# Kernel optimization log

Measured on AMD Instinct MI355X. Metric: run time of the kernel, lower is better.

The kernel has to match this reference:

```python
import jax, jax.numpy as jnp
import numpy as np

CONV_SPECS = [(1, 64, 4, 2), (64, 128, 8, 4), (128, 256, 10, 5), (256, 256, 12, 6)]  # (cin, cout, k, stride)
N_CODEBOOKS = 8
CODEBOOK_SIZE = 1024
D_MODEL = 256
STATE_FRAMES = 4
B = 8192


def setup_inputs() -> dict:
    key = jax.random.key(0)
    ks = jax.random.split(key, 3 + 2 * len(CONV_SPECS) + 1)
    d = {
        "audio_frame": jax.random.normal(ks[0], (B, 1, 240), dtype=jnp.float32),
        "state_in": jax.random.normal(ks[1], (B, D_MODEL, STATE_FRAMES), dtype=jnp.float32),
    }
    for i, (cin, cout, k, s) in enumerate(CONV_SPECS):
        scale = 1.0 / np.sqrt(cin * k)
        d[f"W{i}"] = jax.random.normal(ks[2 + 2 * i], (cout, cin, k), dtype=jnp.float32) * scale
        d[f"b{i}"] = jnp.zeros((cout,), dtype=jnp.float32)
    d["codebooks"] = jax.random.normal(ks[-1], (N_CODEBOOKS, CODEBOOK_SIZE, D_MODEL), dtype=jnp.float32) * 0.02
    return d


def _causal_conv(x, W, b, stride):
    # x: [B, Cin, L]; causal left-pad of (k - stride) so L_out = L // stride
    k = W.shape[-1]
    x = jnp.pad(x, ((0, 0), (0, 0), (k - stride, 0)))
    y = jax.lax.conv_general_dilated(
        x, W, window_strides=(stride,), padding="VALID",
        dimension_numbers=("NCH", "OIH", "NCH"))
    return y + b[None, :, None]


def _rvq_indices(x_btd, codebooks):
    # x_btd: [B, T, D]; codebooks: [Q, K, D] -> indices [B, Q, T]
    r = x_btd
    idxs = []
    for q in range(codebooks.shape[0]):
        cb = codebooks[q]                                        # [K, D]
        # ||r - c||^2 = ||r||^2 - 2 r.c + ||c||^2 ; ||r||^2 constant over k for argmin
        dist = jnp.sum(cb * cb, axis=-1) - 2.0 * jnp.einsum("btd,kd->btk", r, cb)
        idx = jnp.argmin(dist, axis=-1)                          # [B, T]
        r = r - cb[idx]                                          # residual update
        idxs.append(idx)
    return jnp.stack(idxs, axis=1)                               # [B, Q, T]


def reference(audio_frame, state_in, W0, b0, W1, b1, W2, b2, W3, b3, codebooks):
    # state: roll left, zero last frame
    new_state = jnp.roll(state_in, -1, axis=2).at[:, :, -1].set(0.0)

    # causal conv encoder stack (ELU between conv blocks)
    Ws, bs = (W0, W1, W2, W3), (b0, b1, b2, b3)
    x = audio_frame
    for i, (_, _, _, stride) in enumerate(CONV_SPECS):
        x = _causal_conv(x, Ws[i], bs[i], stride)
        if i < len(CONV_SPECS) - 1:
            x = jax.nn.elu(x)
    # x: [B, D_MODEL, 1]

    new_state = new_state.at[:, :, -1].set(x[:, :, -1])

    z = _rvq_indices(x.transpose(0, 2, 1), codebooks)            # [B, Q, T]
    acoustic_tokens = z[:, :, -1]                                # [B, 8]
    return acoustic_tokens, new_state
```

## Files before the change

### kernel.cpp

```cpp
#include <hip/hip_runtime.h>
#include <hip/hip_bf16.h>

#define GB 2

__device__ __forceinline__ float elu1(float v) { return v > 0.f ? v : expm1f(v); }

__global__ void cnorm_kernel(const float* __restrict__ cb, float* __restrict__ cnorm) {
    int g = blockIdx.x * blockDim.x + threadIdx.x;
    if (g >= 8 * 1024) return;
    const float* p = cb + (size_t)g * 256;
    float s = 0.f;
    for (int d = 0; d < 256; d += 4) {
        float4 v = *reinterpret_cast<const float4*>(p + d);
        s += v.x * v.x + v.y * v.y + v.z * v.z + v.w * v.w;
    }
    cnorm[g] = s;
}

__global__ void cbtrans_kernel(const float* __restrict__ cb, float* __restrict__ cbT) {
    int t = blockIdx.x * blockDim.x + threadIdx.x;
    int o = t * 4;
    const int s = o >> 13;
    const int r = o & 8191;
    const int dl = r >> 10;
    const int k = r & 1023;
    const int q = s >> 5;
    const int d = (s & 31) * 8 + dl;
    const float* src = cb + ((size_t)(q * 1024 + k)) * 256 + d;
    float4 v;
    v.x = src[0 * 256]; v.y = src[1 * 256]; v.z = src[2 * 256]; v.w = src[3 * 256];
    *reinterpret_cast<float4*>(cbT + o) = v;
}

__global__ void wtrans_kernel(const float* __restrict__ W1, const float* __restrict__ W2,
                              const float* __restrict__ W3, float* __restrict__ W1T,
                              float* __restrict__ W2T, float* __restrict__ W3T) {
    int g = blockIdx.x * blockDim.x + threadIdx.x;
    if (g < 8192) {
        int ci = g >> 7, c = g & 127;
        const float* src = W1 + c * 512 + ci * 8;
        float4 a = *reinterpret_cast<const float4*>(src);
        float4 b = *reinterpret_cast<const float4*>(src + 4);
        *reinterpret_cast<float4*>(W1T + g * 8) = a;
        *reinterpret_cast<float4*>(W1T + g * 8 + 4) = b;
    }
    int g2 = g - 8192;
    if (g2 >= 0 && g2 < 32768) {
        int ci = g2 >> 8, c = g2 & 255;
        const float* src = W2 + c * 1280 + ci * 10;
        float* dst = W2T + g2 * 10;
#pragma unroll
        for (int j = 0; j < 5; ++j)
            *reinterpret_cast<float2*>(dst + 2 * j) =
                *reinterpret_cast<const float2*>(src + 2 * j);
    }
    int g3 = g - 40960;
    if (g3 >= 0 && g3 < 65536) {
        int ci = g3 >> 8, c = g3 & 255;
        const float* src = W3 + c * 3072 + ci * 12 + 6;
        float* dst = W3T + g3 * 6;
#pragma unroll
        for (int j = 0; j < 3; ++j)
            *reinterpret_cast<float2*>(dst + 2 * j) =
                *reinterpret_cast<const float2*>(src + 2 * j);
    }
}

__global__ __launch_bounds__(256, 2)
void convA_kernel(const float* __restrict__ audio,
                  const float* __restrict__ W0, const float* __restrict__ b0,
                  const float* __restrict__ W1T, const float* __restrict__ b1,
                  float* __restrict__ y1g) {
    __shared__ __align__(16) float xs[244];
    __shared__ __align__(16) float y0s[64 * 124];

    const int tid = threadIdx.x;
    const int b = blockIdx.x;

    if (tid < 64) {
        y0s[tid * 124 + 0] = 0.f; y0s[tid * 124 + 1] = 0.f;
        y0s[tid * 124 + 2] = 0.f; y0s[tid * 124 + 3] = 0.f;
    }
    if (tid < 242) xs[tid] = (tid < 2) ? 0.f : audio[b * 240 + tid - 2];
    __syncthreads();
    {
        const int ci = tid >> 2, tg = tid & 3;
        float4 w = *reinterpret_cast<const float4*>(W0 + ci * 4);
        float bias = b0[ci];
        for (int t = tg; t < 120; t += 4) {
            float v = bias + w.x * xs[2 * t] + w.y * xs[2 * t + 1]
                           + w.z * xs[2 * t + 2] + w.w * xs[2 * t + 3];
            y0s[ci * 124 + 4 + t] = elu1(v);
        }
    }
    __syncthreads();
    {
        const int c = tid >> 1, half = tid & 1, t0 = 15 * half;
        float acc[15];
        float bias = b1[c];
#pragma unroll
        for (int u = 0; u < 15; ++u) acc[u] = bias;
        const float* wbase = W1T + c * 8;
        for (int ci = 0; ci < 64; ++ci) {
            float4 wA = *reinterpret_cast<const float4*>(wbase + ci * 1024);
            float4 wB = *reinterpret_cast<const float4*>(wbase + ci * 1024 + 4);
            const float* yb = y0s + ci * 124 + 4 * t0;
#pragma unroll
            for (int u = 0; u < 15; ++u) {
                float4 a = *reinterpret_cast<const float4*>(yb + 4 * u);
                float4 d = *reinterpret_cast<const float4*>(yb + 4 * u + 4);
                acc[u] += wA.x * a.x + wA.y * a.y + wA.z * a.z + wA.w * a.w
                        + wB.x * d.x + wB.y * d.y + wB.z * d.z + wB.w * d.w;
            }
        }
        float* yo = y1g + ((size_t)b * 128 + c) * 32 + t0;
#pragma unroll
        for (int u = 0; u < 15; ++u) yo[u] = elu1(acc[u]);
    }
}

__global__ __launch_bounds__(256, 2)
void convB_kernel(const float* __restrict__ state_in,
                  const float* __restrict__ b2, const float* __restrict__ b3,
                  const float* __restrict__ W2T, const float* __restrict__ W3T,
                  const float* __restrict__ y1g,
                  float* __restrict__ out, float* __restrict__ r_ws) {
    __shared__ __align__(16) float y1s[GB * 128 * 32];
    __shared__ __align__(16) float y2s[GB * 256 * 6];

    const int tid = threadIdx.x;
    const int bbase = blockIdx.x * GB;

    {
        const int col = tid & 31, grp = tid >> 5;
#pragma unroll
        for (int bi = 0; bi < GB; ++bi) {
            const float* src = y1g + ((size_t)(bbase + bi) * 128 + grp * 16) * 32 + col;
            float* dst = y1s + (bi * 128 + grp * 16) * 32 + col;
#pragma unroll
            for (int i = 0; i < 16; ++i) dst[i * 32] = src[i * 32];
        }
    }
    __syncthreads();
    {
        const int c = tid;
        float acc[GB][6];
        float bias = b2[c];
#pragma unroll
        for (int bi = 0; bi < GB; ++bi)
#pragma unroll
            for (int t = 0; t < 6; ++t) acc[bi][t] = bias;
        const float* wbase = W2T + c * 10;
        for (int ci = 0; ci < 128; ++ci) {
            float w[10];
#pragma unroll
            for (int jj = 0; jj < 5; ++jj) {
                float2 wv = *reinterpret_cast<const float2*>(wbase + ci * 2560 + jj * 2);
                w[jj * 2] = wv.x; w[jj * 2 + 1] = wv.y;
            }
#pragma unroll
            for (int bi = 0; bi < GB; ++bi) {
                const float* yr = y1s + (bi * 128 + ci) * 32;
                float row[32];
#pragma unroll
                for (int k4 = 0; k4 < 8; ++k4) {
                    float4 v = *reinterpret_cast<const float4*>(yr + k4 * 4);
                    row[k4 * 4] = v.x; row[k4 * 4 + 1] = v.y;
                    row[k4 * 4 + 2] = v.z; row[k4 * 4 + 3] = v.w;
                }
                acc[bi][0] += w[5] * row[0] + w[6] * row[1] + w[7] * row[2]
                            + w[8] * row[3] + w[9] * row[4];
#pragma unroll
                for (int t = 1; t < 6; ++t) {
                    const int q0 = 5 * t - 5;
                    float s = 0.f;
#pragma unroll
                    for (int j = 0; j < 10; ++j) s += w[j] * row[q0 + j];
                    acc[bi][t] += s;
                }
            }
        }
#pragma unroll
        for (int bi = 0; bi < GB; ++bi)
#pragma unroll
            for (int t = 0; t < 6; ++t)
                y2s[(bi * 256 + c) * 6 + t] = elu1(acc[bi][t]);
    }
    __syncthreads();
    {
        const int c = tid;
        float acc[GB];
        float bias = b3[c];
#pragma unroll
        for (int bi = 0; bi < GB; ++bi) acc[bi] = bias;
        const float* wbase = W3T + c * 6;
        for (int ci = 0; ci < 256; ++ci) {
            float2 w01 = *reinterpret_cast<const float2*>(wbase + ci * 1536);
            float2 w23 = *reinterpret_cast<const float2*>(wbase + ci * 1536 + 2);
            float2 w45 = *reinterpret_cast<const float2*>(wbase + ci * 1536 + 4);
#pragma unroll
            for (int bi = 0; bi < GB; ++bi) {
                const float* yr = y2s + (bi * 256 + ci) * 6;
                float2 a = *reinterpret_cast<const float2*>(yr);
                float2 d = *reinterpret_cast<const float2*>(yr + 2);
                float2 e = *reinterpret_cast<const float2*>(yr + 4);
                acc[bi] += w01.x * a.x + w01.y * a.y + w23.x * d.x + w23.y * d.y
                         + w45.x * e.x + w45.y * e.y;
            }
        }
#pragma unroll
        for (int bi = 0; bi < GB; ++bi) {
            const int b = bbase + bi;
            float y3 = acc[bi];
            r_ws[b * 256 + c] = y3;
            float4 si = *reinterpret_cast<const float4*>(state_in + b * 1024 + c * 4);
            float4 o; o.x = si.y; o.y = si.z; o.z = si.w; o.w = y3;
            *reinterpret_cast<float4*>(out + 65536 + b * 1024 + c * 4) = o;
        }
    }
}

__device__ __forceinline__ unsigned long long distkey(float d, int k) {
    unsigned u = __float_as_uint(d);
    u = (u & 0x80000000u) ? ~u : (u | 0x80000000u);
    return ((unsigned long long)u << 32) | (unsigned)k;
}

__global__ __launch_bounds__(256)
void rvq_kernel(const float* __restrict__ cb, const float* __restrict__ cbT,
                const float* __restrict__ cnorm, const float* __restrict__ r_ws,
                float* __restrict__ out) {
    __shared__ __align__(16) float rs[16 * 256];
    __shared__ unsigned long long part_sh[2][16];
    __shared__ int idx_sh[16];

    const int tid = threadIdx.x;
    const int lane = tid & 63;
    const int wid = tid >> 6;
    const int bg = wid >> 1;
    const int kg = wid & 1;
    const int b0 = blockIdx.x * 16;
    const int kb = kg * 512 + 4 * lane;

    for (int it = 0; it < 4; ++it) {
        int o = (it * 256 + tid) * 4;
        *reinterpret_cast<float4*>(rs + o) =
            *reinterpret_cast<const float4*>(r_ws + b0 * 256 + o);
    }
    __syncthreads();

    for (int q = 0; q < 8; ++q) {
        float acc[8][8];
#pragma unroll
        for (int i = 0; i < 8; ++i)
#pragma unroll
            for (int j = 0; j < 8; ++j) acc[i][j] = 0.f;

        for (int ds = 0; ds < 32; ++ds) {
            const float* sb = cbT + (size_t)(q * 32 + ds) * 8192;
#pragma unroll
            for (int dp = 0; dp < 2; ++dp) {
                float4 cv0[4], cv1[4];
#pragma unroll
                for (int dd = 0; dd < 4; ++dd) {
                    const int dl = dp * 4 + dd;
                    cv0[dd] = *reinterpret_cast<const float4*>(sb + dl * 1024 + kb);
                    cv1[dd] = *reinterpret_cast<const float4*>(sb + dl * 1024 + kb + 256);
                }
                float rr[8][4];
#pragma unroll
                for (int i = 0; i < 8; ++i) {
                    float4 t = *reinterpret_cast<const float4*>(
                        rs + (bg * 8 + i) * 256 + ds * 8 + dp * 4);
                    rr[i][0] = t.x; rr[i][1] = t.y; rr[i][2] = t.z; rr[i][3] = t.w;
                }
#pragma unroll
                for (int dd = 0; dd < 4; ++dd) {
#pragma unroll
                    for (int i = 0; i < 8; ++i) {
                        const float r = rr[i][dd];
                        acc[i][0] += r * cv0[dd].x; acc[i][1] += r * cv0[dd].y;
                        acc[i][2] += r * cv0[dd].z; acc[i][3] += r * cv0[dd].w;
                        acc[i][4] += r * cv1[dd].x; acc[i][5] += r * cv1[dd].y;
                        acc[i][6] += r * cv1[dd].z; acc[i][7] += r * cv1[dd].w;
                    }
                }
            }
        }
        {
            float4 cn0 = *reinterpret_cast<const float4*>(cnorm + q * 1024 + kb);
            float4 cn1 = *reinterpret_cast<const float4*>(cnorm + q * 1024 + kb + 256);
            float c0e[4] = {cn0.x, cn0.y, cn0.z, cn0.w};
            float c1e[4] = {cn1.x, cn1.y, cn1.z, cn1.w};
#pragma unroll
            for (int i = 0; i < 8; ++i) {
                unsigned long long k = 0xFFFFFFFFFFFFFFFFull;
#pragma unroll
                for (int e = 0; e < 4; ++e) {
                    unsigned long long ka = distkey(c0e[e] - 2.f * acc[i][e], kb + e);
                    unsigned long long kc = distkey(c1e[e] - 2.f * acc[i][4 + e],
                                                    kb + 256 + e);
                    if (ka < k) k = ka;
                    if (kc < k) k = kc;
                }
                for (int off = 32; off >= 1; off >>= 1) {
                    unsigned long long o = __shfl_xor(k, off, 64);
                    if (o < k) k = o;
                }
                if (lane == 0) part_sh[kg][bg * 8 + i] = k;
            }
        }
        __syncthreads();
        if (tid < 16) {
            unsigned long long ka = part_sh[0][tid];
            unsigned long long kc = part_sh[1][tid];
            if (kc < ka) ka = kc;
            const int idx = (int)(ka & 0xFFFFFFFFu);
            idx_sh[tid] = idx;
            out[(b0 + tid) * 8 + q] = (float)idx;
        }
        __syncthreads();
        for (int it = 0; it < 16; ++it) {
            const int idx = idx_sh[it];
            rs[it * 256 + tid] -= cb[((size_t)(q * 1024 + idx)) * 256 + tid];
        }
        __syncthreads();
    }
}

extern "C" void kernel_launch(void* const* d_in, const int* in_sizes, int n_in,
                              void* d_out, int out_size, void* d_ws, size_t ws_size,
                              hipStream_t stream) {
    const float* audio = (const float*)d_in[0];
    const float* state = (const float*)d_in[1];
    const float* W0 = (const float*)d_in[2];
    const float* b0 = (const float*)d_in[3];
    const float* W1 = (const float*)d_in[4];
    const float* b1 = (const float*)d_in[5];
    const float* W2 = (const float*)d_in[6];
    const float* b2 = (const float*)d_in[7];
    const float* W3 = (const float*)d_in[8];
    const float* b3 = (const float*)d_in[9];
    const float* cbk = (const float*)d_in[10];
    float* out = (float*)d_out;

    float* cnorm_ws = (float*)d_ws;
    float* r_ws = cnorm_ws + 8192;
    float* W1T = r_ws + 2097152;
    float* W2T = W1T + 65536;
    float* W3T = W2T + 327680;
    float* y1g = W3T + 393216;
    float* cbT = y1g + 33554432;

    cnorm_kernel<<<32, 256, 0, stream>>>(cbk, cnorm_ws);
    cbtrans_kernel<<<2048, 256, 0, stream>>>(cbk, cbT);
    wtrans_kernel<<<416, 256, 0, stream>>>(W1, W2, W3, W1T, W2T, W3T);
    convA_kernel<<<8192, 256, 0, stream>>>(audio, W0, b0, W1T, b1, y1g);
    convB_kernel<<<8192 / GB, 256, 0, stream>>>(state, b2, b3, W2T, W3T, y1g,
                                                out, r_ws);
    rvq_kernel<<<512, 256, 0, stream>>>(cbk, cbT, cnorm_ws, r_ws, out);
}
```

Baseline: 1.991 ms.

## Remap convB threads to batch x channel-pair and pad transposed weights for float4 loads

Result: slower. 2.257 ms (+13.4%).

```diff
diff --git a/kernel.cpp b/kernel.cpp
--- a/kernel.cpp
+++ b/kernel.cpp
@@ -48,21 +48,23 @@
     if (g2 >= 0 && g2 < 32768) {
         int ci = g2 >> 8, c = g2 & 255;
         const float* src = W2 + c * 1280 + ci * 10;
-        float* dst = W2T + g2 * 10;
+        float* dst = W2T + g2 * 12;
 #pragma unroll
         for (int j = 0; j < 5; ++j)
             *reinterpret_cast<float2*>(dst + 2 * j) =
                 *reinterpret_cast<const float2*>(src + 2 * j);
+        dst[10] = 0.f; dst[11] = 0.f;
     }
     int g3 = g - 40960;
     if (g3 >= 0 && g3 < 65536) {
         int ci = g3 >> 8, c = g3 & 255;
         const float* src = W3 + c * 3072 + ci * 12 + 6;
-        float* dst = W3T + g3 * 6;
+        float* dst = W3T + g3 * 8;
 #pragma unroll
         for (int j = 0; j < 3; ++j)
             *reinterpret_cast<float2*>(dst + 2 * j) =
                 *reinterpret_cast<const float2*>(src + 2 * j);
+        dst[6] = 0.f; dst[7] = 0.f;
     }
 }
 
@@ -130,93 +132,101 @@
 
     const int tid = threadIdx.x;
     const int bbase = blockIdx.x * GB;
+    const int bi = tid >> 7;
+    const int cp = tid & 127;
 
     {
         const int col = tid & 31, grp = tid >> 5;
 #pragma unroll
-        for (int bi = 0; bi < GB; ++bi) {
-            const float* src = y1g + ((size_t)(bbase + bi) * 128 + grp * 16) * 32 + col;
-            float* dst = y1s + (bi * 128 + grp * 16) * 32 + col;
+        for (int b2i = 0; b2i < GB; ++b2i) {
+            const float* src = y1g + ((size_t)(bbase + b2i) * 128 + grp * 16) * 32 + col;
+            float* dst = y1s + (b2i * 128 + grp * 16) * 32 + col;
 #pragma unroll
             for (int i = 0; i < 16; ++i) dst[i * 32] = src[i * 32];
         }
     }
     __syncthreads();
     {
-        const int c = tid;
-        float acc[GB][6];
-        float bias = b2[c];
-#pragma unroll
-        for (int bi = 0; bi < GB; ++bi)
-#pragma unroll
-            for (int t = 0; t < 6; ++t) acc[bi][t] = bias;
-        const float* wbase = W2T + c * 10;
+        float accA[6], accB[6];
+        const float biasA = b2[cp], biasB = b2[cp + 128];
+#pragma unroll
+        for (int t = 0; t < 6; ++t) { accA[t] = biasA; accB[t] = biasB; }
+        const float* ybase = y1s + bi * 128 * 32;
         for (int ci = 0; ci < 128; ++ci) {
-            float w[10];
-#pragma unroll
-            for (int jj = 0; jj < 5; ++jj) {
-                float2 wv = *reinterpret_cast<const float2*>(wbase + ci * 2560 + jj * 2);
-                w[jj * 2] = wv.x; w[jj * 2 + 1] = wv.y;
-            }
-#pragma unroll
-            for (int bi = 0; bi < GB; ++bi) {
-                const float* yr = y1s + (bi * 128 + ci) * 32;
-                float row[32];
-#pragma unroll
-                for (int k4 = 0; k4 < 8; ++k4) {
-                    float4 v = *reinterpret_cast<const float4*>(yr + k4 * 4);
-                    row[k4 * 4] = v.x; row[k4 * 4 + 1] = v.y;
-                    row[k4 * 4 + 2] = v.z; row[k4 * 4 + 3] = v.w;
-                }
-                acc[bi][0] += w[5] * row[0] + w[6] * row[1] + w[7] * row[2]
-                            + w[8] * row[3] + w[9] * row[4];
-#pragma unroll
-                for (int t = 1; t < 6; ++t) {
-                    const int q0 = 5 * t - 5;
-                    float s = 0.f;
-#pragma unroll
-                    for (int j = 0; j < 10; ++j) s += w[j] * row[q0 + j];
-                    acc[bi][t] += s;
-                }
-            }
-        }
-#pragma unroll
-        for (int bi = 0; bi < GB; ++bi)
-#pragma unroll
-            for (int t = 0; t < 6; ++t)
-                y2s[(bi * 256 + c) * 6 + t] = elu1(acc[bi][t]);
-    }
-    __syncthreads();
-    {
-        const int c = tid;
-        float acc[GB];
-        float bias = b3[c];
-#pragma unroll
-        for (int bi = 0; bi < GB; ++bi) acc[bi] = bias;
-        const float* wbase = W3T + c * 6;
+            const float* yr = ybase + ci * 32;
+            float row[32];
+#pragma unroll
+            for (int k4 = 0; k4 < 8; ++k4) {
+                float4 v = *reinterpret_cast<const float4*>(yr + k4 * 4);
+                row[k4 * 4] = v.x; row[k4 * 4 + 1] = v.y;
+                row[k4 * 4 + 2] = v.z; row[k4 * 4 + 3] = v.w;
+            }
+            const float* wpa = W2T + (ci * 256 + cp) * 12;
+            float4 a0 = *reinterpret_cast<const float4*>(wpa);
+            float4 a1 = *reinterpret_cast<const float4*>(wpa + 4);
+            float4 a2 = *reinterpret_cast<const float4*>(wpa + 8);
+            const float* wpb = wpa + 128 * 12;
+            float4 c0 = *reinterpret_cast<const float4*>(wpb);
+            float4 c1 = *reinterpret_cast<const float4*>(wpb + 4);
+            float4 c2 = *reinterpret_cast<const float4*>(wpb + 8);
+            const float wA[10] = {a0.x, a0.y, a0.z, a0.w, a1.x,
+                                  a1.y, a1.z, a1.w, a2.x, a2.y};
+            const float wB[10] = {c0.x, c0.y, c0.z, c0.w, c1.x,
+                                  c1.y, c1.z, c1.w, c2.x, c2.y};
+            accA[0] += wA[5] * row[0] + wA[6] * row[1] + wA[7] * row[2]
+                     + wA[8] * row[3] + wA[9] * row[4];
+            accB[0] += wB[5] * row[0] + wB[6] * row[1] + wB[7] * row[2]
+                     + wB[8] * row[3] + wB[9] * row[4];
+#pragma unroll
+            for (int t = 1; t < 6; ++t) {
+                const int q0 = 5 * t - 5;
+                float sA = 0.f, sB = 0.f;
+#pragma unroll
+                for (int j = 0; j < 10; ++j) {
+                    sA += wA[j] * row[q0 + j];
+                    sB += wB[j] * row[q0 + j];
+                }
+                accA[t] += sA; accB[t] += sB;
+            }
+        }
+        float* yoA = y2s + (bi * 256 + cp) * 6;
+        float* yoB = y2s + (bi * 256 + cp + 128) * 6;
+#pragma unroll
+        for (int t = 0; t < 6; ++t) {
+            yoA[t] = elu1(accA[t]);
+            yoB[t] = elu1(accB[t]);
+        }
+    }
+    __syncthreads();
+    {
+        float accA = b3[cp], accB = b3[cp + 128];
+        const float* ybase = y2s + bi * 256 * 6;
         for (int ci = 0; ci < 256; ++ci) {
-            float2 w01 = *reinterpret_cast<const float2*>(wbase + ci * 1536);
-            float2 w23 = *reinterpret_cast<const float2*>(wbase + ci * 1536 + 2);
-            float2 w45 = *reinterpret_cast<const float2*>(wbase + ci * 1536 + 4);
-#pragma unroll
-            for (int bi = 0; bi < GB; ++bi) {
-                const float* yr = y2s + (bi * 256 + ci) * 6;
-                float2 a = *reinterpret_cast<const float2*>(yr);
-                float2 d = *reinterpret_cast<const float2*>(yr + 2);
-                float2 e = *reinterpret_cast<const float2*>(yr + 4);
-                acc[bi] += w01.x * a.x + w01.y * a.y + w23.x * d.x + w23.y * d.y
-                         + w45.x * e.x + w45.y * e.y;
-            }
-        }
-#pragma unroll
-        for (int bi = 0; bi < GB; ++bi) {
-            const int b = bbase + bi;
-            float y3 = acc[bi];
-            r_ws[b * 256 + c] = y3;
-            float4 si = *reinterpret_cast<const float4*>(state_in + b * 1024 + c * 4);
-            float4 o; o.x = si.y; o.y = si.z; o.z = si.w; o.w = y3;
-            *reinterpret_cast<float4*>(out + 65536 + b * 1024 + c * 4) = o;
-        }
+            const float* yr = ybase + ci * 6;
+            float2 a = *reinterpret_cast<const float2*>(yr);
+            float2 d = *reinterpret_cast<const float2*>(yr + 2);
+            float2 e = *reinterpret_cast<const float2*>(yr + 4);
+            const float* wpa = W3T + (ci * 256 + cp) * 8;
+            float4 wa0 = *reinterpret_cast<const float4*>(wpa);
+            float4 wa1 = *reinterpret_cast<const float4*>(wpa + 4);
+            const float* wpb = wpa + 128 * 8;
+            float4 wb0 = *reinterpret_cast<const float4*>(wpb);
+            float4 wb1 = *reinterpret_cast<const float4*>(wpb + 4);
+            accA += wa0.x * a.x + wa0.y * a.y + wa0.z * d.x + wa0.w * d.y
+                  + wa1.x * e.x + wa1.y * e.y;
+            accB += wb0.x * a.x + wb0.y * a.y + wb0.z * d.x + wb0.w * d.y
+                  + wb1.x * e.x + wb1.y * e.y;
+        }
+        const int b = bbase + bi;
+        r_ws[b * 256 + cp] = accA;
+        r_ws[b * 256 + cp + 128] = accB;
+        float4 siA = *reinterpret_cast<const float4*>(state_in + b * 1024 + cp * 4);
+        float4 oA; oA.x = siA.y; oA.y = siA.z; oA.z = siA.w; oA.w = accA;
+        *reinterpret_cast<float4*>(out + 65536 + b * 1024 + cp * 4) = oA;
+        float4 siB = *reinterpret_cast<const float4*>(
+            state_in + b * 1024 + (cp + 128) * 4);
+        float4 oB; oB.x = siB.y; oB.y = siB.z; oB.z = siB.w; oB.w = accB;
+        *reinterpret_cast<float4*>(out + 65536 + b * 1024 + (cp + 128) * 4) = oB;
     }
 }
 
@@ -348,8 +358,8 @@
     float* r_ws = cnorm_ws + 8192;
     float* W1T = r_ws + 2097152;
     float* W2T = W1T + 65536;
-    float* W3T = W2T + 327680;
-    float* y1g = W3T + 393216;
+    float* W3T = W2T + 393216;
+    float* y1g = W3T + 524288;
     float* cbT = y1g + 33554432;
 
     cnorm_kernel<<<32, 256, 0, stream>>>(cbk, cnorm_ws);
```
